# Kernel tuning notes

Hardware: AMD Instinct MI355X
Metric: run time of the kernel (lower is better)

The kernel has to match this reference:

```python
import jax, jax.numpy as jnp
import numpy as np

TOPK = 2


def setup_inputs() -> dict:
    key = jax.random.key(0)
    k1, k2, k3, k4, k5 = jax.random.split(key, 5)
    D, H, E = 1024, 1408, 8
    hidden_states = jax.random.normal(k1, (2, 1024, D), dtype=jnp.float32)
    gate_w = jax.random.normal(k2, (E, D), dtype=jnp.float32) * 0.02
    w1g = jax.random.normal(k3, (E, D, H), dtype=jnp.float32) * 0.02
    w1u = jax.random.normal(k4, (E, D, H), dtype=jnp.float32) * 0.02
    w2 = jax.random.normal(k5, (E, H, D), dtype=jnp.float32) * 0.02
    return {"hidden_states": hidden_states, "gate_w": gate_w, "w1g": w1g, "w1u": w1u, "w2": w2}


def reference(hidden_states, gate_w, w1g, w1u, w2):
    # hidden_states: [B, S, D]; expert weights: w1g/w1u [E, D, H], w2 [E, H, D]
    B, S, D = hidden_states.shape
    E = gate_w.shape[0]
    x = hidden_states.reshape(-1, D)  # [T, D]
    T = x.shape[0]

    # --- MoEGate: softmax scores, top-k routing (no topk renorm) ---
    logits = x @ gate_w.T                      # [T, E]
    scores = jax.nn.softmax(logits, axis=-1)   # [T, E]
    topk_w, topk_idx = jax.lax.top_k(scores, TOPK)  # [T, K]

    # Per-token combine coefficient for each expert: coeff[t, e] = sum_k w[t,k] * (idx[t,k]==e)
    coeff = jnp.zeros((T, E), dtype=x.dtype).at[jnp.arange(T)[:, None], topk_idx].add(topk_w)

    # --- Grouped expert MLP (swiglu): identical math to permute + grouped GEMM + unpermute ---
    g = jnp.einsum('td,edh->teh', x, w1g)      # [T, E, H]
    u = jnp.einsum('td,edh->teh', x, w1u)      # [T, E, H]
    h = jax.nn.silu(g) * u                     # [T, E, H]
    y = jnp.einsum('teh,te,ehd->td', h, coeff, w2)  # [T, D]
    return y.reshape(B, S, D)
```

## Files before the change

kernel.cpp:

```cpp
#include <hip/hip_runtime.h>

#define TOK 2048
#define DDIM 1024
#define HDIM 1408
#define ENUM 8
#define NSLOT (2 * TOK)
#define UP_NB 22
#define UP_KS 32
#define DN_NB 16
#define DN_KS 44
#define DN_KH 22

typedef unsigned int uint;
typedef unsigned short ushort;

using bf16x8 = __attribute__((ext_vector_type(8))) __bf16;
using f32x4  = __attribute__((ext_vector_type(4))) float;

__device__ __forceinline__ float silu_f(float g) {
    return g / (1.0f + __expf(-g));
}

__device__ __forceinline__ ushort cvt_bf16(float f) {
    uint u = __float_as_uint(f);
    u += 0x7FFFu + ((u >> 16) & 1u);
    return (ushort)(u >> 16);
}

__device__ __forceinline__ void gl2lds16(const void* g, void* l) {
    __builtin_amdgcn_global_load_lds(
        (const __attribute__((address_space(1))) uint*)g,
        (__attribute__((address_space(3))) uint*)l, 16, 0, 0);
}

__global__ __launch_bounds__(64) void gate1_kernel(
    const float* __restrict__ x, const float* __restrict__ gw,
    int* __restrict__ counts, int* __restrict__ toks,
    float* __restrict__ wslot, ushort* __restrict__ xb)
{
    const int t = blockIdx.x;
    const int lane = threadIdx.x;
    const float* xr = x + (size_t)t * DDIM;
    ushort* xbr = xb + (size_t)t * DDIM;
    float xv[16];
#pragma unroll
    for (int i = 0; i < 16; ++i) xv[i] = xr[lane + 64 * i];
#pragma unroll
    for (int i = 0; i < 16; ++i) xbr[lane + 64 * i] = cvt_bf16(xv[i]);
    float logit[ENUM];
#pragma unroll
    for (int e = 0; e < ENUM; ++e) {
        const float* gr = gw + (size_t)e * DDIM;
        float acc = 0.f;
#pragma unroll
        for (int i = 0; i < 16; ++i) acc += xv[i] * gr[lane + 64 * i];
#pragma unroll
        for (int s = 32; s > 0; s >>= 1) acc += __shfl_xor(acc, s, 64);
        logit[e] = acc;
    }
    if (lane == 0) {
        float mx = logit[0];
#pragma unroll
        for (int e = 1; e < ENUM; ++e) mx = fmaxf(mx, logit[e]);
        float p[ENUM]; float se = 0.f;
#pragma unroll
        for (int e = 0; e < ENUM; ++e) { p[e] = __expf(logit[e] - mx); se += p[e]; }
        float inv = 1.0f / se;
#pragma unroll
        for (int e = 0; e < ENUM; ++e) p[e] *= inv;
        int i0 = 0;
#pragma unroll
        for (int e = 1; e < ENUM; ++e) if (p[e] > p[i0]) i0 = e;
        int i1 = (i0 == 0) ? 1 : 0;
#pragma unroll
        for (int e = 0; e < ENUM; ++e) if (e != i0 && p[e] > p[i1]) i1 = e;
        wslot[(t << 1)] = p[i0];
        wslot[(t << 1) | 1] = p[i1];
        int p0 = atomicAdd(&counts[i0], 1);
        toks[i0 * TOK + p0] = (t << 1);
        int p1 = atomicAdd(&counts[i1], 1);
        toks[i1 * TOK + p1] = (t << 1) | 1;
    }
}

__device__ __forceinline__ void tcast64_body(
    const float* __restrict__ src, ushort* __restrict__ dst, int N, int KS, int NB,
    int e, int ks, int nb, int tid)
{
    __shared__ float Ls[32][68];
    const float* st = src + (size_t)e * ((size_t)KS * 32) * N + (size_t)(ks * 32) * N + nb * 64;
    const int n4 = (tid & 15) * 4;
#pragma unroll
    for (int r = 0; r < 2; ++r) {
        int k = (tid >> 4) + r * 16;
        float4 v = *(const float4*)(st + (size_t)k * N + n4);
        Ls[k][n4 + 0] = v.x; Ls[k][n4 + 1] = v.y; Ls[k][n4 + 2] = v.z; Ls[k][n4 + 3] = v.w;
    }
    __syncthreads();

    ushort* dt = dst + ((((size_t)e * NB + nb) * KS) + ks) * 2048;
    const int nn = tid >> 2;
    const int kk0 = (tid & 3) * 8;
    ushort o[8];
#pragma unroll
    for (int j = 0; j < 8; ++j) o[j] = cvt_bf16(Ls[kk0 + j][nn]);
    *(uint4*)(dt + nn * 32 + kk0) = *(uint4*)o;
}

__global__ __launch_bounds__(256) void tcast_all_kernel(
    const float* __restrict__ w1g, const float* __restrict__ w1u,
    const float* __restrict__ w2, ushort* __restrict__ BgP,
    ushort* __restrict__ BuP, ushort* __restrict__ W2P)
{
    const int bid = blockIdx.x;
    const int tid = threadIdx.x;
    if (bid < 16 * 704) {
        const int z = bid / 704;
        const int rem = bid - z * 704;
        const int nb = rem / UP_KS;
        const int ks = rem - nb * UP_KS;
        tcast64_body((z & 8) ? w1u : w1g, (z & 8) ? BuP : BgP,
                     HDIM, UP_KS, UP_NB, z & 7, ks, nb, tid);
    } else {
        const int b2 = bid - 16 * 704;
        const int e = b2 / 704;
        const int rem = b2 - e * 704;
        const int nb = rem / DN_KS;
        const int ks = rem - nb * DN_KS;
        tcast64_body(w2, W2P, DDIM, DN_KS, DN_NB, e, ks, nb, tid);
    }
}

__global__ __launch_bounds__(256, 4) void up_mfma(
    const ushort* __restrict__ xb, const ushort* __restrict__ BgP,
    const ushort* __restrict__ BuP, const int* __restrict__ counts,
    const int* __restrict__ toks, ushort* __restrict__ Hbuf)
{
    const int e = blockIdx.z;
    const int cnt = counts[e];
    const int m0 = blockIdx.y * 128;
    if (m0 >= cnt) return;
    const int nb = blockIdx.x;
    const int tid = threadIdx.x;
    const int w = tid >> 6;
    const int lane = tid & 63;
    const int q = lane >> 4;
    const int l15 = lane & 15;
    const int wr = w >> 1;
    const int wc = w & 1;

    __shared__ ushort As[2][128][32];
    __shared__ ushort Bgs[2][64][32];
    __shared__ ushort Bus[2][64][32];
    __shared__ int rowslot[128];

    if (tid < 128) rowslot[tid] = (m0 + tid < cnt) ? toks[e * TOK + m0 + tid] : -1;
    __syncthreads();

    const int srow = w * 16 + (lane >> 2);
    const int clog = (((lane & 3) + 4 - ((srow >> 1) & 3)) & 3) * 8;
    const int as0 = rowslot[srow];
    const int as1 = rowslot[srow + 64];
    const ushort* agp0 = xb + (size_t)(as0 < 0 ? 0 : (as0 >> 1)) * DDIM + clog;
    const ushort* agp1 = xb + (size_t)(as1 < 0 ? 0 : (as1 >> 1)) * DDIM + clog;
    const size_t tb = (size_t)(e * UP_NB + nb) * UP_KS * 2048;
    const ushort* bgp = BgP + tb + srow * 32 + clog;
    const ushort* bup = BuP + tb + srow * 32 + clog;

    const int coff = ((q + (l15 >> 1)) & 3) * 8;

    f32x4 accg[4][2], accu[4][2];
#pragma unroll
    for (int i = 0; i < 4; ++i)
#pragma unroll
        for (int j = 0; j < 2; ++j) { accg[i][j] = (f32x4)0.f; accu[i][j] = (f32x4)0.f; }

#define UP_PREFETCH(KSV, B)                                        \
    {                                                              \
        gl2lds16(agp0 + (KSV) * 32, &As[B][w * 16][0]);            \
        gl2lds16(agp1 + (KSV) * 32, &As[B][64 + w * 16][0]);       \
        gl2lds16(bgp + (size_t)(KSV) * 2048, &Bgs[B][w * 16][0]);  \
        gl2lds16(bup + (size_t)(KSV) * 2048, &Bus[B][w * 16][0]);  \
    }

    UP_PREFETCH(0, 0);
    __syncthreads();

    for (int ks = 0; ks < UP_KS; ++ks) {
        const int cur = ks & 1;
        const int nxt = cur ^ 1;
        if (ks + 1 < UP_KS) UP_PREFETCH(ks + 1, nxt);

        bf16x8 a[4], bg[2], bu[2];
#pragma unroll
        for (int mi = 0; mi < 4; ++mi)
            a[mi] = *(const bf16x8*)&As[cur][wr * 64 + mi * 16 + l15][coff];
#pragma unroll
        for (int ni = 0; ni < 2; ++ni) {
            bg[ni] = *(const bf16x8*)&Bgs[cur][wc * 32 + ni * 16 + l15][coff];
            bu[ni] = *(const bf16x8*)&Bus[cur][wc * 32 + ni * 16 + l15][coff];
        }
#pragma unroll
        for (int mi = 0; mi < 4; ++mi)
#pragma unroll
            for (int ni = 0; ni < 2; ++ni) {
                accg[mi][ni] = __builtin_amdgcn_mfma_f32_16x16x32_bf16(a[mi], bg[ni], accg[mi][ni], 0, 0, 0);
                accu[mi][ni] = __builtin_amdgcn_mfma_f32_16x16x32_bf16(a[mi], bu[ni], accu[mi][ni], 0, 0, 0);
            }
        __syncthreads();
    }
#undef UP_PREFETCH

#pragma unroll
    for (int mi = 0; mi < 4; ++mi) {
#pragma unroll
        for (int r = 0; r < 4; ++r) {
            int ml = wr * 64 + mi * 16 + q * 4 + r;
            int slot = rowslot[ml];
            if (slot < 0) continue;
            ushort* hrow = Hbuf + (size_t)slot * HDIM + nb * 64 + wc * 32 + l15;
#pragma unroll
            for (int ni = 0; ni < 2; ++ni)
                hrow[ni * 16] = cvt_bf16(silu_f(accg[mi][ni][r]) * accu[mi][ni][r]);
        }
    }
}

__global__ __launch_bounds__(256, 4) void down_mfma(
    const ushort* __restrict__ Hbuf, const ushort* __restrict__ W2P,
    const int* __restrict__ counts, const int* __restrict__ toks,
    float* __restrict__ Ybuf)
{
    const int z = blockIdx.z;
    const int e = z >> 1;
    const int kh = z & 1;
    const int cnt = counts[e];
    const int m0 = blockIdx.y * 128;
    if (m0 >= cnt) return;
    const int nb = blockIdx.x;
    const int tid = threadIdx.x;
    const int w = tid >> 6;
    const int lane = tid & 63;
    const int q = lane >> 4;
    const int l15 = lane & 15;
    const int wr = w >> 1;
    const int wc = w & 1;

    __shared__ ushort As[2][128][32];
    __shared__ ushort Bs[2][128][32];
    __shared__ int rowslot[128];

    if (tid < 128) rowslot[tid] = (m0 + tid < cnt) ? toks[e * TOK + m0 + tid] : -1;
    __syncthreads();

    const int srow = w * 16 + (lane >> 2);
    const int clog = (((lane & 3) + 4 - ((srow >> 1) & 3)) & 3) * 8;
    const int as0 = rowslot[srow];
    const int as1 = rowslot[srow + 64];
    const ushort* agp0 = Hbuf + (size_t)(as0 < 0 ? 0 : as0) * HDIM + kh * (DN_KH * 32) + clog;
    const ushort* agp1 = Hbuf + (size_t)(as1 < 0 ? 0 : as1) * HDIM + kh * (DN_KH * 32) + clog;
    const int nb2 = nb * 2;
    const ushort* bp0 = W2P + ((size_t)(e * DN_NB + nb2) * DN_KS + kh * DN_KH) * 2048 + srow * 32 + clog;
    const ushort* bp1 = W2P + ((size_t)(e * DN_NB + nb2 + 1) * DN_KS + kh * DN_KH) * 2048 + srow * 32 + clog;

    const int coff = ((q + (l15 >> 1)) & 3) * 8;

    f32x4 acc[4][4];
#pragma unroll
    for (int i = 0; i < 4; ++i)
#pragma unroll
        for (int j = 0; j < 4; ++j) acc[i][j] = (f32x4)0.f;

#define DN_PREFETCH(KSV, B)                                           \
    {                                                                 \
        gl2lds16(agp0 + (KSV) * 32, &As[B][w * 16][0]);               \
        gl2lds16(agp1 + (KSV) * 32, &As[B][64 + w * 16][0]);          \
        gl2lds16(bp0 + (size_t)(KSV) * 2048, &Bs[B][w * 16][0]);      \
        gl2lds16(bp1 + (size_t)(KSV) * 2048, &Bs[B][64 + w * 16][0]); \
    }

    DN_PREFETCH(0, 0);
    __syncthreads();

    for (int ks = 0; ks < DN_KH; ++ks) {
        const int cur = ks & 1;
        const int nxt = cur ^ 1;
        if (ks + 1 < DN_KH) DN_PREFETCH(ks + 1, nxt);

        bf16x8 a[4], b[4];
#pragma unroll
        for (int mi = 0; mi < 4; ++mi)
            a[mi] = *(const bf16x8*)&As[cur][wr * 64 + mi * 16 + l15][coff];
#pragma unroll
        for (int ni = 0; ni < 4; ++ni)
            b[ni] = *(const bf16x8*)&Bs[cur][wc * 64 + ni * 16 + l15][coff];
#pragma unroll
        for (int mi = 0; mi < 4; ++mi)
#pragma unroll
            for (int ni = 0; ni < 4; ++ni)
                acc[mi][ni] = __builtin_amdgcn_mfma_f32_16x16x32_bf16(a[mi], b[ni], acc[mi][ni], 0, 0, 0);
        __syncthreads();
    }
#undef DN_PREFETCH

    float* Yp = Ybuf + (size_t)kh * NSLOT * DDIM;
#pragma unroll
    for (int mi = 0; mi < 4; ++mi) {
#pragma unroll
        for (int r = 0; r < 4; ++r) {
            int ml = wr * 64 + mi * 16 + q * 4 + r;
            int slot = rowslot[ml];
            if (slot < 0) continue;
            float* yr = Yp + (size_t)slot * DDIM + nb * 128 + wc * 64 + l15;
#pragma unroll
            for (int ni = 0; ni < 4; ++ni)
                yr[ni * 16] = acc[mi][ni][r];
        }
    }
}

__global__ __launch_bounds__(256) void combine_kernel(
    const float* __restrict__ Ybuf, const float* __restrict__ wslot,
    float* __restrict__ y)
{
    const int t = blockIdx.x;
    const int j = threadIdx.x * 4;
    const float w0 = wslot[2 * t];
    const float w1 = wslot[2 * t + 1];
    const float* y00 = Ybuf + ((size_t)2 * t) * DDIM + j;
    const float* y01 = Ybuf + ((size_t)2 * t + 1) * DDIM + j;
    const float* y10 = y00 + (size_t)NSLOT * DDIM;
    const float* y11 = y01 + (size_t)NSLOT * DDIM;
    float4 a0 = *(const float4*)y00;
    float4 b0 = *(const float4*)y01;
    float4 a1 = *(const float4*)y10;
    float4 b1 = *(const float4*)y11;
    float4 o;
    o.x = w0 * (a0.x + a1.x) + w1 * (b0.x + b1.x);
    o.y = w0 * (a0.y + a1.y) + w1 * (b0.y + b1.y);
    o.z = w0 * (a0.z + a1.z) + w1 * (b0.z + b1.z);
    o.w = w0 * (a0.w + a1.w) + w1 * (b0.w + b1.w);
    *(float4*)(y + (size_t)t * DDIM + j) = o;
}

extern "C" void kernel_launch(void* const* d_in, const int* in_sizes, int n_in,
                              void* d_out, int out_size, void* d_ws, size_t ws_size,
                              hipStream_t stream) {
    const float* x   = (const float*)d_in[0];
    const float* gw  = (const float*)d_in[1];
    const float* w1g = (const float*)d_in[2];
    const float* w1u = (const float*)d_in[3];
    const float* w2  = (const float*)d_in[4];
    float* y = (float*)d_out;
    char* ws = (char*)d_ws;

    size_t off = 0;
    int*    counts = (int*)(ws + off);   off += 256;
    int*    toks   = (int*)(ws + off);   off += (size_t)ENUM * TOK * 4;
    float*  wslot  = (float*)(ws + off); off += (size_t)NSLOT * 4;
    off = (off + 255) & ~(size_t)255;
    ushort* xb     = (ushort*)(ws + off); off += (size_t)TOK * DDIM * 2;
    size_t regA = off;
    ushort* BgP  = (ushort*)(ws + regA);
    ushort* BuP  = (ushort*)(ws + regA + (size_t)ENUM * DDIM * HDIM * 2);
    float*  Ybuf = (float*)(ws + regA);
    off = regA + (size_t)2 * ENUM * DDIM * HDIM * 2;
    ushort* W2P  = (ushort*)(ws + off);  off += (size_t)ENUM * HDIM * DDIM * 2;
    ushort* Hbuf = (ushort*)(ws + off);

    hipMemsetAsync(counts, 0, ENUM * sizeof(int), stream);
    gate1_kernel<<<TOK, 64, 0, stream>>>(x, gw, counts, toks, wslot, xb);
    tcast_all_kernel<<<16896, 256, 0, stream>>>(w1g, w1u, w2, BgP, BuP, W2P);

    up_mfma<<<dim3(UP_NB, TOK / 128, ENUM), 256, 0, stream>>>(xb, BgP, BuP, counts, toks, Hbuf);
    down_mfma<<<dim3(DDIM / 128, TOK / 128, 16), 256, 0, stream>>>(Hbuf, W2P, counts, toks, Ybuf);
    combine_kernel<<<TOK, 256, 0, stream>>>(Ybuf, wslot, y);
}
```

Measured before the change: 298.0 us.

## Fold routing bucketing into weight-cast kernel and coarsen cast blocks

Gate kernel now writes a packed top-2 expert id per token instead of doing global atomics, and the memset is removed. The token bucketing moves into extra blocks of the weight-cast kernel, which count with shared-memory atomics. Each cast block now handles four K-slices instead of one, so there are four times fewer blocks, and the LDS row is padded to 69. This saves one memset launch and global atomic contention, and cuts block scheduling overhead. The trade-off is serialized work per block, and the order of tokens within each expert changes.

```diff
diff --git a/kernel.cpp b/kernel.cpp
--- a/kernel.cpp
+++ b/kernel.cpp
@@ -10,6 +10,8 @@
 #define DN_NB 16
 #define DN_KS 44
 #define DN_KH 22
+#define TC_W1_BLK 2816
+#define TC_ALL_BLK 4224
 
 typedef unsigned int uint;
 typedef unsigned short ushort;
@@ -35,8 +37,7 @@
 
 __global__ __launch_bounds__(64) void gate1_kernel(
     const float* __restrict__ x, const float* __restrict__ gw,
-    int* __restrict__ counts, int* __restrict__ toks,
-    float* __restrict__ wslot, ushort* __restrict__ xb)
+    int* __restrict__ tinfo, float* __restrict__ wslot, ushort* __restrict__ xb)
 {
     const int t = blockIdx.x;
     const int lane = threadIdx.x;
@@ -74,60 +75,76 @@
         int i1 = (i0 == 0) ? 1 : 0;
 #pragma unroll
         for (int e = 0; e < ENUM; ++e) if (e != i0 && p[e] > p[i1]) i1 = e;
+        tinfo[t] = i0 | (i1 << 4);
         wslot[(t << 1)] = p[i0];
         wslot[(t << 1) | 1] = p[i1];
-        int p0 = atomicAdd(&counts[i0], 1);
-        toks[i0 * TOK + p0] = (t << 1);
-        int p1 = atomicAdd(&counts[i1], 1);
-        toks[i1 * TOK + p1] = (t << 1) | 1;
-    }
-}
-
-__device__ __forceinline__ void tcast64_body(
-    const float* __restrict__ src, ushort* __restrict__ dst, int N, int KS, int NB,
-    int e, int ks, int nb, int tid)
-{
-    __shared__ float Ls[32][68];
-    const float* st = src + (size_t)e * ((size_t)KS * 32) * N + (size_t)(ks * 32) * N + nb * 64;
-    const int n4 = (tid & 15) * 4;
-#pragma unroll
-    for (int r = 0; r < 2; ++r) {
-        int k = (tid >> 4) + r * 16;
-        float4 v = *(const float4*)(st + (size_t)k * N + n4);
-        Ls[k][n4 + 0] = v.x; Ls[k][n4 + 1] = v.y; Ls[k][n4 + 2] = v.z; Ls[k][n4 + 3] = v.w;
-    }
-    __syncthreads();
-
-    ushort* dt = dst + ((((size_t)e * NB + nb) * KS) + ks) * 2048;
-    const int nn = tid >> 2;
-    const int kk0 = (tid & 3) * 8;
-    ushort o[8];
-#pragma unroll
-    for (int j = 0; j < 8; ++j) o[j] = cvt_bf16(Ls[kk0 + j][nn]);
-    *(uint4*)(dt + nn * 32 + kk0) = *(uint4*)o;
+    }
 }
 
 __global__ __launch_bounds__(256) void tcast_all_kernel(
     const float* __restrict__ w1g, const float* __restrict__ w1u,
     const float* __restrict__ w2, ushort* __restrict__ BgP,
-    ushort* __restrict__ BuP, ushort* __restrict__ W2P)
+    ushort* __restrict__ BuP, ushort* __restrict__ W2P,
+    const int* __restrict__ tinfo, int* __restrict__ counts,
+    int* __restrict__ toks)
 {
     const int bid = blockIdx.x;
     const int tid = threadIdx.x;
-    if (bid < 16 * 704) {
-        const int z = bid / 704;
-        const int rem = bid - z * 704;
-        const int nb = rem / UP_KS;
-        const int ks = rem - nb * UP_KS;
-        tcast64_body((z & 8) ? w1u : w1g, (z & 8) ? BuP : BgP,
-                     HDIM, UP_KS, UP_NB, z & 7, ks, nb, tid);
+
+    __shared__ float Ls[32][69];
+    __shared__ int cnt;
+
+    if (bid >= TC_ALL_BLK) {
+        const int e = bid - TC_ALL_BLK;
+        if (tid == 0) cnt = 0;
+        __syncthreads();
+        for (int t = tid; t < TOK; t += 256) {
+            int info = tinfo[t];
+            if ((info & 15) == e) { int p = atomicAdd(&cnt, 1); toks[e * TOK + p] = (t << 1); }
+            if ((info >> 4) == e) { int p = atomicAdd(&cnt, 1); toks[e * TOK + p] = (t << 1) | 1; }
+        }
+        __syncthreads();
+        if (tid == 0) counts[e] = cnt;
+        return;
+    }
+
+    const float* src; ushort* dst; int N, KS, NB, e, nb, ks0;
+    if (bid < TC_W1_BLK) {
+        const int z = bid / 176;
+        const int rem = bid - z * 176;
+        src = (z & 8) ? w1u : w1g;
+        dst = (z & 8) ? BuP : BgP;
+        N = HDIM; KS = UP_KS; NB = UP_NB; e = z & 7;
+        nb = rem >> 3; ks0 = (rem & 7) * 4;
     } else {
-        const int b2 = bid - 16 * 704;
-        const int e = b2 / 704;
-        const int rem = b2 - e * 704;
-        const int nb = rem / DN_KS;
-        const int ks = rem - nb * DN_KS;
-        tcast64_body(w2, W2P, DDIM, DN_KS, DN_NB, e, ks, nb, tid);
+        const int b2 = bid - TC_W1_BLK;
+        e = b2 / 176;
+        const int rem = b2 - e * 176;
+        src = w2; dst = W2P;
+        N = DDIM; KS = DN_KS; NB = DN_NB;
+        nb = rem / 11; ks0 = (rem - nb * 11) * 4;
+    }
+
+    const int n4 = (tid & 15) * 4;
+    const int nn = tid >> 2;
+    const int kk0 = (tid & 3) * 8;
+
+    for (int ksi = 0; ksi < 4; ++ksi) {
+        const int ks = ks0 + ksi;
+        const float* st = src + (size_t)e * ((size_t)KS * 32) * N + (size_t)(ks * 32) * N + nb * 64;
+#pragma unroll
+        for (int r = 0; r < 2; ++r) {
+            int k = (tid >> 4) + r * 16;
+            float4 v = *(const float4*)(st + (size_t)k * N + n4);
+            Ls[k][n4 + 0] = v.x; Ls[k][n4 + 1] = v.y; Ls[k][n4 + 2] = v.z; Ls[k][n4 + 3] = v.w;
+        }
+        __syncthreads();
+        ushort* dt = dst + ((((size_t)e * NB + nb) * KS) + ks) * 2048;
+        ushort o[8];
+#pragma unroll
+        for (int j = 0; j < 8; ++j) o[j] = cvt_bf16(Ls[kk0 + j][nn]);
+        *(uint4*)(dt + nn * 32 + kk0) = *(uint4*)o;
+        __syncthreads();
     }
 }
 
@@ -358,6 +375,7 @@
     int*    counts = (int*)(ws + off);   off += 256;
     int*    toks   = (int*)(ws + off);   off += (size_t)ENUM * TOK * 4;
     float*  wslot  = (float*)(ws + off); off += (size_t)NSLOT * 4;
+    int*    tinfo  = (int*)(ws + off);   off += (size_t)TOK * 4;
     off = (off + 255) & ~(size_t)255;
     ushort* xb     = (ushort*)(ws + off); off += (size_t)TOK * DDIM * 2;
     size_t regA = off;
@@ -368,9 +386,9 @@
     ushort* W2P  = (ushort*)(ws + off);  off += (size_t)ENUM * HDIM * DDIM * 2;
     ushort* Hbuf = (ushort*)(ws + off);
 
-    hipMemsetAsync(counts, 0, ENUM * sizeof(int), stream);
-    gate1_kernel<<<TOK, 64, 0, stream>>>(x, gw, counts, toks, wslot, xb);
-    tcast_all_kernel<<<16896, 256, 0, stream>>>(w1g, w1u, w2, BgP, BuP, W2P);
+    gate1_kernel<<<TOK, 64, 0, stream>>>(x, gw, tinfo, wslot, xb);
+    tcast_all_kernel<<<TC_ALL_BLK + ENUM, 256, 0, stream>>>(
+        w1g, w1u, w2, BgP, BuP, W2P, tinfo, counts, toks);
 
     up_mfma<<<dim3(UP_NB, TOK / 128, ENUM), 256, 0, stream>>>(xb, BgP, BuP, counts, toks, Hbuf);
     down_mfma<<<dim3(DDIM / 128, TOK / 128, 16), 256, 0, stream>>>(Hbuf, W2P, counts, toks, Ybuf);
```

New measurement: 259.7 us. 12.8% less time.
